# Kernel optimization log

Measured on AMD Instinct MI355X. Metric: run time of the kernel, lower is better.

Reference implementation:

```python
import jax, jax.numpy as jnp
import numpy as np

B, L, N, P = 64, 512, 321, 720   # batch, seq_len, enc_in, pred_len
E, R, CID, H = 8, 32, 32, 64     # experts, rank, channel_identity_dim, router hidden


def setup_inputs() -> dict:
    key = jax.random.key(0)
    ks = jax.random.split(key, 9)
    return {
        "x": jax.random.normal(ks[0], (B, L, N), dtype=jnp.float32),
        # per-channel identity embedding for the router
        "ident": jax.random.normal(ks[1], (N, CID), dtype=jnp.float32) * 0.02,
        # router MLP: CID -> H -> E
        "rw1": jax.random.normal(ks[2], (CID, H), dtype=jnp.float32) * (1.0 / np.sqrt(CID)),
        "rb1": jnp.zeros((H,), dtype=jnp.float32),
        "rw2": jax.random.normal(ks[3], (H, E), dtype=jnp.float32) * (1.0 / np.sqrt(H)),
        "rb2": jnp.zeros((E,), dtype=jnp.float32),
        # low-rank experts: L -> R -> P
        "w1": jax.random.normal(ks[4], (E, L, R), dtype=jnp.float32) * (1.0 / np.sqrt(L)),
        "w2": jax.random.normal(ks[5], (E, R, P), dtype=jnp.float32) * (1.0 / np.sqrt(R)),
        "b": jnp.zeros((E, P), dtype=jnp.float32),
    }


def reference(x, ident, rw1, rb1, rw2, rb2, w1, w2, b):
    # RevIN-style normalization over the time dim (torch std is unbiased, ddof=1)
    mean = jnp.mean(x, axis=1, keepdims=True)                    # [B,1,N]
    std = jnp.std(x, axis=1, keepdims=True, ddof=1) + 1e-6       # [B,1,N]
    xn = ((x - mean) / std).transpose(0, 2, 1)                   # [B,N,L]

    # per-channel MoE router (soft routing over experts)
    hidden = jax.nn.relu(ident @ rw1 + rb1)                      # [N,H]
    gate = jax.nn.softmax(hidden @ rw2 + rb2, axis=-1)           # [N,E]

    # low-rank expert projections L -> R -> P
    h = jnp.einsum('bnl,elr->bner', xn, w1)                      # [B,N,E,R]
    y = jnp.einsum('bner,erp->bnep', h, w2) + b                  # [B,N,E,P]
    y = jnp.einsum('bnep,ne->bnp', y, gate)                      # [B,N,P]

    pred = y.transpose(0, 2, 1)                                  # [B,P,N]
    return pred * std + mean
```

## Files before the change

### kernel.cpp

```cpp
#include <hip/hip_runtime.h>
#include <math.h>

#define B_ 64
#define L_ 512
#define N_ 321
#define P_ 720
#define E_ 8
#define R_ 32
#define CID_ 32
#define H_ 64
#define ER_ 256
#define KB2 288
#define HGROWS 384

typedef __attribute__((ext_vector_type(8))) short bf16x8;
typedef __attribute__((ext_vector_type(4))) float f32x4;
typedef __attribute__((ext_vector_type(8))) unsigned short u16x8;
typedef __attribute__((ext_vector_type(4))) unsigned short u16x4;

#define OFF_GATE 0
#define OFF_CS1  2568
#define OFF_W1K  2824
#define OFF_W2X  68360
#define OFF_HG   172040

__device__ __forceinline__ unsigned short f2bf(float f) {
    unsigned u = __float_as_uint(f);
    u += 0x7fffu + ((u >> 16) & 1u);
    return (unsigned short)(u >> 16);
}
__device__ __forceinline__ float bf2f(unsigned short h) {
    return __uint_as_float(((unsigned)h) << 16);
}

__global__ void prep_kernel(const float* __restrict__ w1, const float* __restrict__ w2,
                            const float* __restrict__ bias,
                            const float* __restrict__ ident,
                            const float* __restrict__ rw1, const float* __restrict__ rb1,
                            const float* __restrict__ rw2, const float* __restrict__ rb2,
                            unsigned short* __restrict__ w1k, unsigned short* __restrict__ w2x,
                            float* __restrict__ cs1, float* __restrict__ gate) {
    __shared__ float red[16][32];
    __shared__ float hid[H_];
    __shared__ float lg[E_];
    int bid = blockIdx.x, t = threadIdx.x;
    if (bid < 128) {
        #pragma unroll
        for (int r = 0; r < 2; ++r) {
            int g = bid*1024 + r*512 + t;
            int er = g >> 9, l = g & 511;
            w1k[g] = f2bf(w1[(size_t)(er >> 5)*(L_*R_) + (size_t)l*R_ + (er & 31)]);
        }
    } else if (bid < 848) {
        int p = bid - 128;
        if (t < KB2) {
            unsigned short v;
            if (t < ER_)            v = f2bf(w2[(size_t)t*P_ + p]);
            else if (t < ER_ + E_)  v = f2bf(bias[(size_t)(t - ER_)*P_ + p]);
            else if (t == ER_ + E_) v = 0x3f80;
            else                    v = 0;
            w2x[(size_t)p*KB2 + t] = v;
        }
    } else if (bid < 856) {
        int e = bid - 848;
        int q = t >> 5, r = t & 31;
        float s = 0.f;
        for (int l = q; l < L_; l += 16)
            s += bf2f(f2bf(w1[(size_t)e*(L_*R_) + (size_t)l*R_ + r]));
        red[q][r] = s;
        __syncthreads();
        if (q == 0) {
            #pragma unroll
            for (int qq = 1; qq < 16; ++qq) s += red[qq][r];
            cs1[e*32 + r] = s;
        }
    } else {
        int n = bid - 856;
        if (t < H_) {
            float acc = rb1[t];
            #pragma unroll
            for (int c = 0; c < CID_; ++c)
                acc = fmaf(ident[n*CID_ + c], rw1[c*H_ + t], acc);
            hid[t] = fmaxf(acc, 0.f);
        }
        __syncthreads();
        if (t < E_) {
            float a = rb2[t];
            #pragma unroll
            for (int h = 0; h < H_; ++h) a = fmaf(hid[h], rw2[h*E_ + t], a);
            lg[t] = a;
        }
        __syncthreads();
        if (t == 0) {
            float m = lg[0];
            #pragma unroll
            for (int e = 1; e < E_; ++e) m = fmaxf(m, lg[e]);
            float s = 0.f, ex[E_];
            #pragma unroll
            for (int e = 0; e < E_; ++e) { ex[e] = expf(lg[e] - m); s += ex[e]; }
            float inv = 1.f / s;
            #pragma unroll
            for (int e = 0; e < E_; ++e) gate[n*E_ + e] = ex[e] * inv;
        }
    }
}

__global__ __launch_bounds__(512, 4) void gemm1_kernel(
        const float* __restrict__ x, const unsigned short* __restrict__ w1k,
        const float* __restrict__ gate, const float* __restrict__ cs1,
        unsigned short* __restrict__ hg) {
    __shared__ unsigned short buf[2][64][128];
    __shared__ float red1[8][64], red2[8][64];
    __shared__ float meanS[64], sdS[64];

    const int bid = blockIdx.x;
    const int xcd = bid & 7;
    const int idx = bid >> 3;
    const int b   = (xcd << 3) + idx / 12;
    const int rem = idx % 12;
    const int nt  = rem >> 1;
    const int eq  = rem & 1;
    const int n0  = nt * 64;
    const int m0  = eq * 128;

    const int tid  = threadIdx.x;
    const int lane = tid & 63;
    const int wave = tid >> 6;
    const int l15  = lane & 15;
    const int kgrp = lane >> 4;

    const int xn  = lane;
    const int gn  = n0 + xn;
    const int gnc = (gn < N_) ? gn : (N_ - 1);
    const float* xp = x + (size_t)b*L_*N_ + gnc;
    const int swz = (xn & 7) << 4;
    char* myrow0 = (char*)&buf[0][xn][0];
    char* myrow1 = (char*)&buf[1][xn][0];

    const unsigned short* apA = w1k + (size_t)(m0 + wave*16 + l15)*L_;
    const int rsw = (l15 & 7) << 4;

    float s1 = 0.f, s2 = 0.f;
    float v[16];
    f32x4 acc[4];
    #pragma unroll
    for (int j = 0; j < 4; ++j) acc[j] = (f32x4){0.f,0.f,0.f,0.f};

#define LOADV(rd_) {                                                            \
    const int kb = (rd_)*128 + wave*16;                                         \
    _Pragma("unroll")                                                           \
    for (int i_ = 0; i_ < 16; ++i_)                                             \
        v[i_] = xp[(size_t)(kb + i_)*N_]; }
#define STOREV(rd_) {                                                           \
    char* dst = ((rd_) & 1) ? myrow1 : myrow0;                                  \
    u16x8 pk0, pk1;                                                             \
    _Pragma("unroll")                                                           \
    for (int i_ = 0; i_ < 8; ++i_) {                                            \
        s1 += v[i_]; s2 = fmaf(v[i_], v[i_], s2); pk0[i_] = f2bf(v[i_]); }      \
    _Pragma("unroll")                                                           \
    for (int i_ = 0; i_ < 8; ++i_) {                                            \
        float f_ = v[8+i_];                                                     \
        s1 += f_; s2 = fmaf(f_, f_, s2); pk1[i_] = f2bf(f_); }                  \
    *(u16x8*)(dst + ((wave*32)      ^ swz)) = pk0;                              \
    *(u16x8*)(dst + ((wave*32 + 16) ^ swz)) = pk1; }

    LOADV(0);
    STOREV(0);
    __syncthreads();

    bf16x8 af[4];
#define LDA(s_, kk_) af[s_] = *(const bf16x8*)&apA[(kk_)*32 + kgrp*8];
    LDA(0, 0); LDA(1, 1);

    #pragma unroll
    for (int rd = 0; rd < 4; ++rd) {
        if (rd < 3) LOADV(rd + 1);
        const unsigned short (*cb)[128] = buf[rd & 1];
        #pragma unroll
        for (int ks = 0; ks < 4; ++ks) {
            const int kk = rd*4 + ks;
            if (kk + 2 < 16) LDA((kk + 2) & 3, kk + 2);
            const int cbyte = ks*64 + kgrp*16;
            bf16x8 bfr[4];
            #pragma unroll
            for (int fn = 0; fn < 4; ++fn)
                bfr[fn] = *(const bf16x8*)((const char*)&cb[fn*16 + l15][0] + (cbyte ^ rsw));
            #pragma unroll
            for (int fn = 0; fn < 4; ++fn)
                acc[fn] = __builtin_amdgcn_mfma_f32_16x16x32_bf16(af[kk & 3], bfr[fn], acc[fn], 0, 0, 0);
        }
        if (rd < 3) STOREV(rd + 1);
        __syncthreads();
    }
#undef LDA
#undef LOADV
#undef STOREV

    red1[wave][xn] = s1;
    red2[wave][xn] = s2;
    __syncthreads();
    if (tid < 64) {
        float a = 0.f, qq = 0.f;
        #pragma unroll
        for (int kk = 0; kk < 8; ++kk) { a += red1[kk][tid]; qq += red2[kk][tid]; }
        float mean = a * (1.f/L_);
        float var = (qq - (float)L_*mean*mean) * (1.f/(L_-1));
        var = fmaxf(var, 0.f);
        meanS[tid] = mean;
        sdS[tid]   = sqrtf(var) + 1e-6f;
    }
    __syncthreads();

    unsigned short* hgb = hg + ((size_t)b * HGROWS + n0) * KB2;
    {
        int er0 = m0 + wave*16 + kgrp*4;
        int e = er0 >> 5;
        f32x4 c4 = *(const f32x4*)&cs1[er0];
        #pragma unroll
        for (int fn = 0; fn < 4; ++fn) {
            int nl = fn*16 + l15;
            int gnn = n0 + nl; if (gnn > N_-1) gnn = N_-1;
            float g = gate[gnn*E_ + e];
            float m = meanS[nl];
            u16x4 pk;
            #pragma unroll
            for (int j = 0; j < 4; ++j)
                pk[j] = f2bf(g * (acc[fn][j] - m * c4[j]));
            *(u16x4*)&hgb[(size_t)nl*KB2 + er0] = pk;
        }
    }
    if (eq == 1) {
        int nl = tid >> 3, seg = tid & 7;
        int gnn = n0 + nl; if (gnn > N_-1) gnn = N_-1;
        float sd = sdS[nl], m = meanS[nl];
        u16x4 pk;
        #pragma unroll
        for (int jj = 0; jj < 4; ++jj) {
            int k = seg*4 + jj;
            float vv = (k < E_) ? gate[gnn*E_ + k] * sd : ((k == E_) ? m : 0.f);
            pk[jj] = f2bf(vv);
        }
        *(u16x4*)&hgb[(size_t)nl*KB2 + ER_ + seg*4] = pk;
    }
}

#define HGS 296
__global__ __launch_bounds__(512, 6) void gemm2_kernel(
        const unsigned short* __restrict__ hg, const unsigned short* __restrict__ w2x,
        float* __restrict__ out) {
    __shared__ __align__(16) char smem[64 * HGS * 2];
    unsigned short* hgL = (unsigned short*)smem;
    const int bid = blockIdx.x;
    const int xcd = bid & 7;
    const int idx = bid >> 3;
    const int b   = (xcd << 3) + idx / 36;
    const int rem = idx % 36;
    const int p0  = (rem / 6) * 128;
    const int n0  = (rem % 6) * 64;

    const int tid  = threadIdx.x;
    const int lane = tid & 63;
    const int wave = tid >> 6;
    const int l15  = lane & 15;
    const int kgrp = lane >> 4;

    const unsigned short* hgb = hg + ((size_t)b * HGROWS + n0) * KB2;
    #pragma unroll
    for (int it = 0; it < 5; ++it) {
        int c = tid + it*512;
        if (c < 64*36) {
            int row = c / 36, col = c % 36;
            *(u16x8*)&hgL[(size_t)row*HGS + col*8] =
                *(const u16x8*)&hgb[(size_t)row*KB2 + col*8];
        }
    }
    __syncthreads();

    int prow = p0 + wave*16 + l15; if (prow > P_-1) prow = P_-1;
    const unsigned short* ap = w2x + (size_t)prow*KB2;
    f32x4 o[4];
    #pragma unroll
    for (int j = 0; j < 4; ++j) o[j] = (f32x4){0.f,0.f,0.f,0.f};
    #pragma unroll
    for (int ks = 0; ks < 9; ++ks) {
        bf16x8 afr = *(const bf16x8*)&ap[ks*32 + kgrp*8];
        #pragma unroll
        for (int fn = 0; fn < 4; ++fn) {
            bf16x8 bfr = *(const bf16x8*)&hgL[(size_t)(fn*16 + l15)*HGS + ks*32 + kgrp*8];
            o[fn] = __builtin_amdgcn_mfma_f32_16x16x32_bf16(afr, bfr, o[fn], 0, 0, 0);
        }
    }
    __syncthreads();

    float* patch = (float*)smem + wave * 1088;
    #pragma unroll
    for (int fn = 0; fn < 4; ++fn)
        #pragma unroll
        for (int j = 0; j < 4; ++j)
            patch[(kgrp*4 + j)*68 + fn*16 + l15] = o[fn][j];
    const int pw0 = p0 + wave*16;
    #pragma unroll
    for (int pass = 0; pass < 4; ++pass) {
        int ploc = pass*4 + kgrp;
        f32x4 v = *(const f32x4*)&patch[ploc*68 + l15*4];
        int p = pw0 + ploc;
        int n = n0 + l15*4;
        if (p < P_) {
            float* orow = out + ((size_t)b*P_ + p)*N_;
            if (n + 3 < N_) {
                *(f32x4*)&orow[n] = v;
            } else {
                #pragma unroll
                for (int j = 0; j < 4; ++j)
                    if (n + j < N_) orow[n + j] = v[j];
            }
        }
    }
}

extern "C" void kernel_launch(void* const* d_in, const int* in_sizes, int n_in,
                              void* d_out, int out_size, void* d_ws, size_t ws_size,
                              hipStream_t stream) {
    const float* x     = (const float*)d_in[0];
    const float* ident = (const float*)d_in[1];
    const float* rw1   = (const float*)d_in[2];
    const float* rb1   = (const float*)d_in[3];
    const float* rw2   = (const float*)d_in[4];
    const float* rb2   = (const float*)d_in[5];
    const float* w1    = (const float*)d_in[6];
    const float* w2    = (const float*)d_in[7];
    const float* bias  = (const float*)d_in[8];
    float* out = (float*)d_out;
    float* ws  = (float*)d_ws;

    float* gate = ws + OFF_GATE;
    float* cs1  = ws + OFF_CS1;
    unsigned short* w1k = (unsigned short*)(ws + OFF_W1K);
    unsigned short* w2x = (unsigned short*)(ws + OFF_W2X);
    unsigned short* hg  = (unsigned short*)(ws + OFF_HG);

    prep_kernel<<<856 + N_, 512, 0, stream>>>(w1, w2, bias, ident, rw1, rb1,
                                              rw2, rb2, w1k, w2x, cs1, gate);
    gemm1_kernel<<<dim3(768), 512, 0, stream>>>(x, w1k, gate, cs1, hg);
    gemm2_kernel<<<dim3(2304), 512, 0, stream>>>(hg, w2x, out);
}
```

Measured before the change: 59.60 us.

## Warp-specialize gemm1 into producer and MFMA consumer waves over full ER tile

gemm1 now gives each block all 256 expert-rank rows for a 64-channel tile, halving the grid and removing the duplicate read and normalization-statistics pass over x that the two eq halves used to do. Four producer waves stream x from global into double-buffered LDS as bf16 while accumulating the sums, and four consumer waves each compute a 64x64 tile with 16 accumulators via MFMA. The aim is to cut redundant x traffic and overlap loads with compute. In exchange, per-thread register use rises (v[32] and 16 accumulators), half the waves are idle during the MFMA phase, and only 384 blocks are launched, which may leave the GPU under-occupied.

```diff
diff --git a/kernel.cpp b/kernel.cpp
--- a/kernel.cpp
+++ b/kernel.cpp
@@ -110,99 +110,99 @@
         const float* __restrict__ gate, const float* __restrict__ cs1,
         unsigned short* __restrict__ hg) {
     __shared__ unsigned short buf[2][64][128];
-    __shared__ float red1[8][64], red2[8][64];
+    __shared__ float red1[4][64], red2[4][64];
     __shared__ float meanS[64], sdS[64];
 
     const int bid = blockIdx.x;
     const int xcd = bid & 7;
     const int idx = bid >> 3;
-    const int b   = (xcd << 3) + idx / 12;
-    const int rem = idx % 12;
-    const int nt  = rem >> 1;
-    const int eq  = rem & 1;
-    const int n0  = nt * 64;
-    const int m0  = eq * 128;
+    const int b   = (xcd << 3) + idx / 6;
+    const int n0  = (idx % 6) * 64;
 
     const int tid  = threadIdx.x;
     const int lane = tid & 63;
     const int wave = tid >> 6;
     const int l15  = lane & 15;
     const int kgrp = lane >> 4;
-
-    const int xn  = lane;
-    const int gn  = n0 + xn;
+    const bool producer = (wave < 4);
+
+    const int kq  = wave & 3;
+    const int gn  = n0 + lane;
     const int gnc = (gn < N_) ? gn : (N_ - 1);
     const float* xp = x + (size_t)b*L_*N_ + gnc;
-    const int swz = (xn & 7) << 4;
-    char* myrow0 = (char*)&buf[0][xn][0];
-    char* myrow1 = (char*)&buf[1][xn][0];
-
-    const unsigned short* apA = w1k + (size_t)(m0 + wave*16 + l15)*L_;
+    const int swz = (lane & 7) << 4;
+
+    const int cw  = wave - 4;
     const int rsw = (l15 & 7) << 4;
 
     float s1 = 0.f, s2 = 0.f;
-    float v[16];
-    f32x4 acc[4];
-    #pragma unroll
-    for (int j = 0; j < 4; ++j) acc[j] = (f32x4){0.f,0.f,0.f,0.f};
+    float v[32];
+    f32x4 acc[4][4];
+    #pragma unroll
+    for (int i = 0; i < 4; ++i)
+        #pragma unroll
+        for (int j = 0; j < 4; ++j) acc[i][j] = (f32x4){0.f,0.f,0.f,0.f};
+    bf16x8 af[2][4];
 
 #define LOADV(rd_) {                                                            \
-    const int kb = (rd_)*128 + wave*16;                                         \
+    const int kb = (rd_)*128 + kq*32;                                           \
     _Pragma("unroll")                                                           \
-    for (int i_ = 0; i_ < 16; ++i_)                                             \
-        v[i_] = xp[(size_t)(kb + i_)*N_]; }
-#define STOREV(rd_) {                                                           \
-    char* dst = ((rd_) & 1) ? myrow1 : myrow0;                                  \
-    u16x8 pk0, pk1;                                                             \
+    for (int i_ = 0; i_ < 32; ++i_)                                             \
+        v[i_] = xp[(size_t)(kb + i_)*N_];                                       \
+    __builtin_amdgcn_sched_barrier(0); }
+#define STOREV(nb_) {                                                           \
+    char* dst = (char*)&buf[nb_][lane][0];                                      \
     _Pragma("unroll")                                                           \
-    for (int i_ = 0; i_ < 8; ++i_) {                                            \
-        s1 += v[i_]; s2 = fmaf(v[i_], v[i_], s2); pk0[i_] = f2bf(v[i_]); }      \
+    for (int j_ = 0; j_ < 4; ++j_) {                                            \
+        u16x8 pk;                                                               \
+        _Pragma("unroll")                                                       \
+        for (int q_ = 0; q_ < 8; ++q_) {                                        \
+            float f_ = v[j_*8 + q_];                                            \
+            s1 += f_; s2 = fmaf(f_, f_, s2); pk[q_] = f2bf(f_); }               \
+        *(u16x8*)(dst + ((kq*64 + j_*16) ^ swz)) = pk; } }
+#define LDAX(s_, kk_) {                                                         \
     _Pragma("unroll")                                                           \
-    for (int i_ = 0; i_ < 8; ++i_) {                                            \
-        float f_ = v[8+i_];                                                     \
-        s1 += f_; s2 = fmaf(f_, f_, s2); pk1[i_] = f2bf(f_); }                  \
-    *(u16x8*)(dst + ((wave*32)      ^ swz)) = pk0;                              \
-    *(u16x8*)(dst + ((wave*32 + 16) ^ swz)) = pk1; }
-
-    LOADV(0);
-    STOREV(0);
-    __syncthreads();
-
-    bf16x8 af[4];
-#define LDA(s_, kk_) af[s_] = *(const bf16x8*)&apA[(kk_)*32 + kgrp*8];
-    LDA(0, 0); LDA(1, 1);
+    for (int fm_ = 0; fm_ < 4; ++fm_)                                           \
+        af[s_][fm_] = *(const bf16x8*)&w1k[(size_t)(cw*64 + fm_*16 + l15)*L_    \
+                                           + (kk_)*32 + kgrp*8]; }
+
+    if (producer) { LOADV(0); STOREV(0); }
+    else          { LDAX(0, 0); }
+    __syncthreads();
 
     #pragma unroll
     for (int rd = 0; rd < 4; ++rd) {
-        if (rd < 3) LOADV(rd + 1);
-        const unsigned short (*cb)[128] = buf[rd & 1];
-        #pragma unroll
-        for (int ks = 0; ks < 4; ++ks) {
-            const int kk = rd*4 + ks;
-            if (kk + 2 < 16) LDA((kk + 2) & 3, kk + 2);
-            const int cbyte = ks*64 + kgrp*16;
-            bf16x8 bfr[4];
-            #pragma unroll
-            for (int fn = 0; fn < 4; ++fn)
-                bfr[fn] = *(const bf16x8*)((const char*)&cb[fn*16 + l15][0] + (cbyte ^ rsw));
-            #pragma unroll
-            for (int fn = 0; fn < 4; ++fn)
-                acc[fn] = __builtin_amdgcn_mfma_f32_16x16x32_bf16(af[kk & 3], bfr[fn], acc[fn], 0, 0, 0);
-        }
-        if (rd < 3) STOREV(rd + 1);
+        if (producer) {
+            if (rd < 3) { LOADV(rd + 1); STOREV((rd + 1) & 1); }
+        } else {
+            #pragma unroll
+            for (int ks = 0; ks < 4; ++ks) {
+                const int kk = rd*4 + ks;
+                if (kk + 1 < 16) LDAX((kk + 1) & 1, kk + 1);
+                const int cbyte = ks*64 + kgrp*16;
+                bf16x8 bfr[4];
+                #pragma unroll
+                for (int fn = 0; fn < 4; ++fn)
+                    bfr[fn] = *(const bf16x8*)((const char*)&buf[rd & 1][fn*16 + l15][0] + (cbyte ^ rsw));
+                #pragma unroll
+                for (int fm = 0; fm < 4; ++fm)
+                    #pragma unroll
+                    for (int fn = 0; fn < 4; ++fn)
+                        acc[fm][fn] = __builtin_amdgcn_mfma_f32_16x16x32_bf16(af[kk & 1][fm], bfr[fn], acc[fm][fn], 0, 0, 0);
+            }
+        }
         __syncthreads();
     }
-#undef LDA
 #undef LOADV
 #undef STOREV
-
-    red1[wave][xn] = s1;
-    red2[wave][xn] = s2;
+#undef LDAX
+
+    if (producer) { red1[kq][lane] = s1; red2[kq][lane] = s2; }
     __syncthreads();
     if (tid < 64) {
         float a = 0.f, qq = 0.f;
         #pragma unroll
-        for (int kk = 0; kk < 8; ++kk) { a += red1[kk][tid]; qq += red2[kk][tid]; }
+        for (int kk = 0; kk < 4; ++kk) { a += red1[kk][tid]; qq += red2[kk][tid]; }
         float mean = a * (1.f/L_);
         float var = (qq - (float)L_*mean*mean) * (1.f/(L_-1));
         var = fmaxf(var, 0.f);
@@ -212,35 +212,41 @@
     __syncthreads();
 
     unsigned short* hgb = hg + ((size_t)b * HGROWS + n0) * KB2;
-    {
-        int er0 = m0 + wave*16 + kgrp*4;
-        int e = er0 >> 5;
-        f32x4 c4 = *(const f32x4*)&cs1[er0];
-        #pragma unroll
-        for (int fn = 0; fn < 4; ++fn) {
-            int nl = fn*16 + l15;
-            int gnn = n0 + nl; if (gnn > N_-1) gnn = N_-1;
-            float g = gate[gnn*E_ + e];
-            float m = meanS[nl];
-            u16x4 pk;
-            #pragma unroll
-            for (int j = 0; j < 4; ++j)
-                pk[j] = f2bf(g * (acc[fn][j] - m * c4[j]));
-            *(u16x4*)&hgb[(size_t)nl*KB2 + er0] = pk;
-        }
-    }
-    if (eq == 1) {
-        int nl = tid >> 3, seg = tid & 7;
+    if (!producer) {
+        #pragma unroll
+        for (int fm = 0; fm < 4; ++fm) {
+            int er0 = cw*64 + fm*16 + kgrp*4;
+            int e = er0 >> 5;
+            f32x4 c4 = *(const f32x4*)&cs1[er0];
+            #pragma unroll
+            for (int fn = 0; fn < 4; ++fn) {
+                int nl = fn*16 + l15;
+                int gnn = n0 + nl; if (gnn > N_-1) gnn = N_-1;
+                float g = gate[gnn*E_ + e];
+                float m = meanS[nl];
+                u16x4 pk;
+                #pragma unroll
+                for (int j = 0; j < 4; ++j)
+                    pk[j] = f2bf(g * (acc[fm][fn][j] - m * c4[j]));
+                *(u16x4*)&hgb[(size_t)nl*KB2 + er0] = pk;
+            }
+        }
+    } else {
+        int nl = tid >> 2, sg = tid & 3;
         int gnn = n0 + nl; if (gnn > N_-1) gnn = N_-1;
         float sd = sdS[nl], m = meanS[nl];
-        u16x4 pk;
-        #pragma unroll
-        for (int jj = 0; jj < 4; ++jj) {
-            int k = seg*4 + jj;
-            float vv = (k < E_) ? gate[gnn*E_ + k] * sd : ((k == E_) ? m : 0.f);
-            pk[jj] = f2bf(vv);
-        }
-        *(u16x4*)&hgb[(size_t)nl*KB2 + ER_ + seg*4] = pk;
+        #pragma unroll
+        for (int h = 0; h < 2; ++h) {
+            int seg = sg*2 + h;
+            u16x4 pk;
+            #pragma unroll
+            for (int jj = 0; jj < 4; ++jj) {
+                int k = seg*4 + jj;
+                float vv = (k < E_) ? gate[gnn*E_ + k] * sd : ((k == E_) ? m : 0.f);
+                pk[jj] = f2bf(vv);
+            }
+            *(u16x4*)&hgb[(size_t)nl*KB2 + ER_ + seg*4] = pk;
+        }
     }
 }
 
@@ -341,6 +347,6 @@
 
     prep_kernel<<<856 + N_, 512, 0, stream>>>(w1, w2, bias, ident, rw1, rb1,
                                               rw2, rb2, w1k, w2x, cs1, gate);
-    gemm1_kernel<<<dim3(768), 512, 0, stream>>>(x, w1k, gate, cs1, hg);
+    gemm1_kernel<<<dim3(384), 512, 0, stream>>>(x, w1k, gate, cs1, hg);
     gemm2_kernel<<<dim3(2304), 512, 0, stream>>>(hg, w2x, out);
 }
```

Measured after the change: 65.01 us. 1.09x slower.
